# Optimization experiments

Measured on AMD Instinct MI355X. Metric: run time of the kernel, lower is better.

Reference implementation:

```python
import jax, jax.numpy as jnp
import numpy as np

N, C, H, W = 1024, 16, 32, 32
E = 4096


def setup_inputs() -> dict:
    key = jax.random.key(0)
    ks = jax.random.split(key, 10)
    feats = jax.random.normal(ks[0], (N, C, H, W), dtype=jnp.float32)
    src = jax.random.randint(ks[1], (E,), 0, N)
    dst = jax.random.randint(ks[2], (E,), 0, N)
    sign = jax.random.randint(ks[3], (E,), 0, 2) * 2 - 1  # values in {-1, +1}
    edges = jnp.stack([src, sign, dst], axis=1).astype(jnp.int64)
    s = 0.05
    w1 = jax.random.normal(ks[4], (2 * C, 3 * C, 3, 3), dtype=jnp.float32) * s
    b1 = jnp.zeros((2 * C,), dtype=jnp.float32)
    w2 = jax.random.normal(ks[5], (2 * C, 2 * C, 3, 3), dtype=jnp.float32) * s
    b2 = jnp.zeros((2 * C,), dtype=jnp.float32)
    w3 = jax.random.normal(ks[6], (C, 2 * C, 3, 3), dtype=jnp.float32) * s
    b3 = jnp.zeros((C,), dtype=jnp.float32)
    return {"feats": feats, "edges": edges, "w1": w1, "b1": b1,
            "w2": w2, "b2": b2, "w3": w3, "b3": b3}


def _pool_edges(edges, feats, positive):
    # Bidirectional gather + scatter_add over selected edges.
    # Mask-by-zero keeps shapes static (equivalent math to torch.where selection).
    sign = edges[:, 1]
    mask = (sign > 0) if positive else (sign < 0)
    w = mask.astype(feats.dtype)[:, None, None, None]
    src = edges[:, 0]
    dst = edges[:, 2]
    pooled = jnp.zeros_like(feats)
    pooled = pooled.at[dst].add(feats[src] * w)  # src -> dst
    pooled = pooled.at[src].add(feats[dst] * w)  # dst -> src
    return pooled


def _conv(x, w, b):
    y = jax.lax.conv_general_dilated(
        x, w, window_strides=(1, 1), padding=((1, 1), (1, 1)),
        dimension_numbers=("NCHW", "OIHW", "NCHW"))
    return y + b[None, :, None, None]


def _leaky(x):
    return jax.nn.leaky_relu(x, negative_slope=0.1)


def reference(feats, edges, w1, b1, w2, b2, w3, b3):
    pos = _pool_edges(edges, feats, positive=True)
    neg = _pool_edges(edges, feats, positive=False)
    x = jnp.concatenate([feats, pos, neg], axis=1)  # [N, 3C, H, W]
    x = _leaky(_conv(x, w1, b1))
    x = _leaky(_conv(x, w2, b2))
    x = _leaky(_conv(x, w3, b3))
    return x
```

## Files before the change

kernel.cpp:

```cpp
#include <hip/hip_runtime.h>


#define NIMG 1024
#define CHW  16384
#define NEDGE 4096
#define MAXD 64

#define ICP1 56
#define ICP2 40
#define XSZ (34*34*ICP1)
#define WSZ (14*32*32)

#define WG1N (14*32*32)
#define WG2N (9*32*32)
#define WG3N (9*16*32)
#define WGTOT (WG1N+WG2N+WG3N)

typedef __attribute__((ext_vector_type(8))) _Float16 half8;
typedef __attribute__((ext_vector_type(4))) _Float16 half4;
typedef __attribute__((ext_vector_type(4))) float float4v;

__device__ __forceinline__ float leaky(float x) { return x > 0.f ? x : 0.1f * x; }

__global__ __launch_bounds__(256) void prep_kernel(
    const float* __restrict__ feats, _Float16* __restrict__ fcl,
    const int* __restrict__ edges, int* __restrict__ deg, int* __restrict__ adj,
    const float* __restrict__ w1, const float* __restrict__ w2,
    const float* __restrict__ w3, _Float16* __restrict__ wg)
{
    __shared__ int sdeg[NIMG];
    const int b = blockIdx.x, tid = threadIdx.x;
    if (b < NIMG) {
        const int n = b;
        const float* fb = feats + (size_t)n * CHW;
        _Float16*    ob = fcl   + (size_t)n * 1024 * 16;
        const int p0 = tid * 4;
        float4v t[16];
        #pragma unroll
        for (int c = 0; c < 16; ++c) t[c] = *(const float4v*)(fb + (c << 10) + p0);
        #pragma unroll
        for (int u = 0; u < 4; ++u) {
            half8 v0, v1;
            #pragma unroll
            for (int c = 0; c < 8; ++c) { v0[c] = (_Float16)t[c][u]; v1[c] = (_Float16)t[c+8][u]; }
            *(half8*)(ob + (p0+u)*16)     = v0;
            *(half8*)(ob + (p0+u)*16 + 8) = v1;
        }
        return;
    }
    for (int i = tid; i < NIMG; i += 256) sdeg[i] = 0;
    __syncthreads();
    const bool is64 = (edges[1] == 0);
    for (int it = 0; it < NEDGE/256; ++it) {
        const int e = it*256 + tid;
        int s, sg, d;
        if (is64) { s = edges[6*e]; sg = edges[6*e + 2]; d = edges[6*e + 4]; }
        else      { s = edges[3*e]; sg = edges[3*e + 1]; d = edges[3*e + 2]; }
        const int tag_d = (d << 1) | (int)(sg > 0);
        const int tag_s = (s << 1) | (int)(sg > 0);
        int i = atomicAdd(&sdeg[s], 1); if (i < MAXD) adj[(s << 6) + i] = tag_d;
        int j = atomicAdd(&sdeg[d], 1); if (j < MAXD) adj[(d << 6) + j] = tag_s;
    }
    __syncthreads();
    for (int i = tid; i < NIMG; i += 256) deg[i] = sdeg[i];

    for (int t = tid; t < WGTOT; t += 256) {
        _Float16 val = (_Float16)0.f;
        if (t < WG1N) {
            int ks = t >> 10, oc = (t >> 5) & 31, j32 = t & 31;
            int k = ks*32 + j32;
            if (k < 432) { int tap = k / 48, ic = k - tap*48;
                           val = (_Float16)w1[(oc*48 + ic)*9 + tap]; }
        } else if (t < WG1N + WG2N) {
            int u = t - WG1N;
            int ks = u >> 10, oc = (u >> 5) & 31, j32 = u & 31;
            int k = ks*32 + j32;
            int tap = k >> 5, ic = k & 31;
            val = (_Float16)w2[(oc*32 + ic)*9 + tap];
        } else {
            int u = t - (WG1N + WG2N);
            int ks = u >> 9, oc = (u >> 5) & 15, j32 = u & 31;
            int k = ks*32 + j32;
            int tap = k >> 5, ic = k & 31;
            val = (_Float16)w3[(oc*32 + ic)*9 + tap];
        }
        wg[t] = val;
    }
}

__global__ __launch_bounds__(512, 2) void conv_kernel(
    const _Float16* __restrict__ fcl,
    const int* __restrict__ deg, const int* __restrict__ adj,
    const _Float16* __restrict__ wg,
    const float* __restrict__ b1, const float* __restrict__ b2,
    const float* __restrict__ b3, float* __restrict__ out)
{
    __shared__ __align__(16) _Float16 Xs[XSZ];
    __shared__ __align__(16) _Float16 Ws[WSZ];
    const int n    = blockIdx.x;
    const int tid  = threadIdx.x;
    const int wave = tid >> 6;
    const int lane = tid & 63;
    const int col  = lane & 15;
    const int quad = lane >> 4;

    {
        const half8* fc = (const half8*)(fcl + (size_t)n * CHW);
        int m = deg[n]; if (m > MAXD) m = MAXD;
        const int* al = adj + (n << 6);
        #pragma unroll 2
        for (int h = 0; h < 2; ++h) {
            const int p = tid + h*512;
            const int base = (((p >> 5) + 1)*34 + (p & 31) + 1) * ICP1;
            *(half8*)(Xs + base)     = fc[2*p];
            *(half8*)(Xs + base + 8) = fc[2*p + 1];
            float ap[16], an[16];
            #pragma unroll
            for (int c = 0; c < 16; ++c) { ap[c] = 0.f; an[c] = 0.f; }
            int i = 0;
            for (; i + 8 <= m; i += 8) {
                int v[8]; half8 x[16];
                #pragma unroll
                for (int u = 0; u < 8; ++u) v[u] = al[i+u];
                #pragma unroll
                for (int u = 0; u < 8; ++u) {
                    const half8* f = (const half8*)(fcl + (size_t)(v[u] >> 1) * CHW);
                    x[2*u] = f[2*p]; x[2*u+1] = f[2*p+1];
                }
                #pragma unroll
                for (int u = 0; u < 8; ++u) {
                    if (v[u] & 1) { for (int c = 0; c < 8; ++c) { ap[c] += (float)x[2*u][c]; ap[c+8] += (float)x[2*u+1][c]; } }
                    else          { for (int c = 0; c < 8; ++c) { an[c] += (float)x[2*u][c]; an[c+8] += (float)x[2*u+1][c]; } }
                }
            }
            for (; i + 4 <= m; i += 4) {
                int v[4]; half8 x[8];
                #pragma unroll
                for (int u = 0; u < 4; ++u) v[u] = al[i+u];
                #pragma unroll
                for (int u = 0; u < 4; ++u) {
                    const half8* f = (const half8*)(fcl + (size_t)(v[u] >> 1) * CHW);
                    x[2*u] = f[2*p]; x[2*u+1] = f[2*p+1];
                }
                #pragma unroll
                for (int u = 0; u < 4; ++u) {
                    if (v[u] & 1) { for (int c = 0; c < 8; ++c) { ap[c] += (float)x[2*u][c]; ap[c+8] += (float)x[2*u+1][c]; } }
                    else          { for (int c = 0; c < 8; ++c) { an[c] += (float)x[2*u][c]; an[c+8] += (float)x[2*u+1][c]; } }
                }
            }
            for (; i < m; ++i) {
                const int v = al[i];
                const half8* fb = (const half8*)(fcl + (size_t)(v >> 1) * CHW);
                half8 x0 = fb[2*p], x1 = fb[2*p + 1];
                if (v & 1) {
                    #pragma unroll
                    for (int c = 0; c < 8; ++c) { ap[c] += (float)x0[c]; ap[c+8] += (float)x1[c]; }
                } else {
                    #pragma unroll
                    for (int c = 0; c < 8; ++c) { an[c] += (float)x0[c]; an[c+8] += (float)x1[c]; }
                }
            }
            half8 h0, h1, h2, h3;
            #pragma unroll
            for (int c = 0; c < 8; ++c) { h0[c] = (_Float16)ap[c]; h1[c] = (_Float16)ap[c+8];
                                          h2[c] = (_Float16)an[c]; h3[c] = (_Float16)an[c+8]; }
            *(half8*)(Xs + base + 16) = h0;
            *(half8*)(Xs + base + 24) = h1;
            *(half8*)(Xs + base + 32) = h2;
            *(half8*)(Xs + base + 40) = h3;
        }
        {
            const half8* src = (const half8*)wg;
            half8* dst = (half8*)Ws;
            for (int t = tid; t < WG1N/8; t += 512) dst[t] = src[t];
        }
        if (tid < 132) {
            int hp, wp;
            if      (tid < 34)  { hp = 0;        wp = tid; }
            else if (tid < 68)  { hp = 33;       wp = tid - 34; }
            else if (tid < 100) { hp = tid - 67; wp = 0; }
            else                { hp = tid - 99; wp = 33; }
            int hb = (hp*34 + wp) * ICP1;
            #pragma unroll
            for (int t = 0; t < 6; ++t) *(half8*)(Xs + hb + t*8) = (half8)0;
        }
    }
    __syncthreads();

    float4v acc[2][8];

    {
        #pragma unroll
        for (int m = 0; m < 2; ++m)
            #pragma unroll
            for (int j = 0; j < 8; ++j) acc[m][j] = (float4v){0.f,0.f,0.f,0.f};
        int pixb[8];
        #pragma unroll
        for (int j = 0; j < 8; ++j) {
            int p = wave*128 + j*16 + col;
            pixb[j] = ((p >> 5)*34 + (p & 31)) * ICP1;
        }
        const int abase = col*32 + quad*8;
        #pragma unroll
        for (int ks = 0; ks < 14; ++ks) {
            int kq  = ks*32 + quad*8;
            int tap = kq / 48;
            int off = 0;
            if (tap < 9) {
                int ic0 = kq - tap*48;
                int dh = tap / 3, dw = tap - dh*3;
                off = (dh*34 + dw)*ICP1 + ic0;
            }
            half8 a0 = *(const half8*)(Ws + ks*1024 + abase);
            half8 a1 = *(const half8*)(Ws + ks*1024 + 512 + abase);
            #pragma unroll
            for (int j = 0; j < 8; ++j) {
                half8 b = *(const half8*)(Xs + pixb[j] + off);
                acc[0][j] = __builtin_amdgcn_mfma_f32_16x16x32_f16(a0, b, acc[0][j], 0, 0, 0);
                acc[1][j] = __builtin_amdgcn_mfma_f32_16x16x32_f16(a1, b, acc[1][j], 0, 0, 0);
            }
        }
    }
    __syncthreads();

    {
        if (tid < 132) {
            int hp, wp;
            if      (tid < 34)  { hp = 0;        wp = tid; }
            else if (tid < 68)  { hp = 33;       wp = tid - 34; }
            else if (tid < 100) { hp = tid - 67; wp = 0; }
            else                { hp = tid - 99; wp = 33; }
            int hb = (hp*34 + wp) * ICP2;
            #pragma unroll
            for (int t = 0; t < 4; ++t) *(half8*)(Xs + hb + t*8) = (half8)0;
        }
        float bv[2][4];
        #pragma unroll
        for (int m = 0; m < 2; ++m)
            #pragma unroll
            for (int r = 0; r < 4; ++r) bv[m][r] = b1[m*16 + quad*4 + r];
        #pragma unroll
        for (int m = 0; m < 2; ++m)
            #pragma unroll
            for (int j = 0; j < 8; ++j) {
                int p = wave*128 + j*16 + col;
                _Float16* y = Xs + ((((p>>5)+1)*34) + (p&31) + 1)*ICP2 + m*16 + quad*4;
                half4 v;
                #pragma unroll
                for (int r = 0; r < 4; ++r) v[r] = (_Float16)leaky(acc[m][j][r] + bv[m][r]);
                *(half4*)y = v;
            }
        {
            const half8* src = (const half8*)(wg + WG1N);
            half8* dst = (half8*)Ws;
            for (int t = tid; t < WG2N/8; t += 512) dst[t] = src[t];
        }
    }
    __syncthreads();

    {
        #pragma unroll
        for (int m = 0; m < 2; ++m)
            #pragma unroll
            for (int j = 0; j < 8; ++j) acc[m][j] = (float4v){0.f,0.f,0.f,0.f};
        int pixb[8];
        #pragma unroll
        for (int j = 0; j < 8; ++j) {
            int p = wave*128 + j*16 + col;
            pixb[j] = ((p >> 5)*34 + (p & 31)) * ICP2;
        }
        const int abase = col*32 + quad*8;
        #pragma unroll
        for (int ks = 0; ks < 9; ++ks) {
            int kq  = ks*32 + quad*8;
            int tap = kq >> 5, ic0 = kq & 31;
            int dh = tap / 3, dw = tap - dh*3;
            int off = (dh*34 + dw)*ICP2 + ic0;
            half8 a0 = *(const half8*)(Ws + ks*1024 + abase);
            half8 a1 = *(const half8*)(Ws + ks*1024 + 512 + abase);
            #pragma unroll
            for (int j = 0; j < 8; ++j) {
                half8 b = *(const half8*)(Xs + pixb[j] + off);
                acc[0][j] = __builtin_amdgcn_mfma_f32_16x16x32_f16(a0, b, acc[0][j], 0, 0, 0);
                acc[1][j] = __builtin_amdgcn_mfma_f32_16x16x32_f16(a1, b, acc[1][j], 0, 0, 0);
            }
        }
    }
    __syncthreads();

    {
        float bv[2][4];
        #pragma unroll
        for (int m = 0; m < 2; ++m)
            #pragma unroll
            for (int r = 0; r < 4; ++r) bv[m][r] = b2[m*16 + quad*4 + r];
        #pragma unroll
        for (int m = 0; m < 2; ++m)
            #pragma unroll
            for (int j = 0; j < 8; ++j) {
                int p = wave*128 + j*16 + col;
                _Float16* y = Xs + ((((p>>5)+1)*34) + (p&31) + 1)*ICP2 + m*16 + quad*4;
                half4 v;
                #pragma unroll
                for (int r = 0; r < 4; ++r) v[r] = (_Float16)leaky(acc[m][j][r] + bv[m][r]);
                *(half4*)y = v;
            }
        {
            const half8* src = (const half8*)(wg + WG1N + WG2N);
            half8* dst = (half8*)Ws;
            for (int t = tid; t < WG3N/8; t += 512) dst[t] = src[t];
        }
    }
    __syncthreads();

    {
        float4v a3[8];
        #pragma unroll
        for (int j = 0; j < 8; ++j) a3[j] = (float4v){0.f,0.f,0.f,0.f};
        int pixb[8];
        #pragma unroll
        for (int j = 0; j < 8; ++j) {
            int p = wave*128 + j*16 + col;
            pixb[j] = ((p >> 5)*34 + (p & 31)) * ICP2;
        }
        const int abase = col*32 + quad*8;
        #pragma unroll
        for (int ks = 0; ks < 9; ++ks) {
            int kq  = ks*32 + quad*8;
            int tap = kq >> 5, ic0 = kq & 31;
            int dh = tap / 3, dw = tap - dh*3;
            int off = (dh*34 + dw)*ICP2 + ic0;
            half8 a0 = *(const half8*)(Ws + ks*512 + abase);
            #pragma unroll
            for (int j = 0; j < 8; ++j) {
                half8 b = *(const half8*)(Xs + pixb[j] + off);
                a3[j] = __builtin_amdgcn_mfma_f32_16x16x32_f16(a0, b, a3[j], 0, 0, 0);
            }
        }
        float bv[4];
        #pragma unroll
        for (int r = 0; r < 4; ++r) bv[r] = b3[quad*4 + r];
        float* op = out + (size_t)n * CHW;
        #pragma unroll
        for (int j = 0; j < 8; ++j) {
            int p = wave*128 + j*16 + col;
            #pragma unroll
            for (int r = 0; r < 4; ++r)
                op[(quad*4 + r)*1024 + p] = leaky(a3[j][r] + bv[r]);
        }
    }
}

extern "C" void kernel_launch(void* const* d_in, const int* in_sizes, int n_in,
                              void* d_out, int out_size, void* d_ws, size_t ws_size,
                              hipStream_t stream) {
    const float* feats = (const float*)d_in[0];
    const int*   edges = (const int*)  d_in[1];
    const float* w1 = (const float*)d_in[2];
    const float* b1 = (const float*)d_in[3];
    const float* w2 = (const float*)d_in[4];
    const float* b2 = (const float*)d_in[5];
    const float* w3 = (const float*)d_in[6];
    const float* b3 = (const float*)d_in[7];
    float* out = (float*)d_out;

    _Float16* fcl = (_Float16*)d_ws;
    int* deg = (int*)((char*)d_ws + (32u << 20));
    int* adj = deg + NIMG;
    _Float16* wg = (_Float16*)((char*)d_ws + (32u << 20) + 4096 + NIMG*MAXD*4);

    prep_kernel<<<dim3(NIMG + 1), dim3(256), 0, stream>>>(
        feats, fcl, edges, deg, adj, w1, w2, w3, wg);
    conv_kernel<<<dim3(NIMG), dim3(512), 0, stream>>>(fcl, deg, adj, wg,
                                                      b1, b2, b3, out);
}
```

Baseline: 268.2 us.

## Overlap neighbor gather with self-channel conv1 MFMAs and drop weight LDS staging

Reorders the conv1 K dimension so the first five k-steps use only the image's own channels. Those MFMAs now run while the first batch of neighbor gathers is in flight, and the pooled channels are written afterwards. Conv weights are read directly from global memory instead of being staged in LDS, which frees about 28 KB of shared memory. Edge adjacency building is spread over 16 blocks using global atomics after a memset, replacing a single block doing all edges serially. The cost is an extra memset launch, more register pressure from the prefetched gather data, and a small padding increase in conv1 from 14 to 15 k-steps.

After: 221.6 us. 1.21x faster.

```diff
diff --git a/kernel.cpp b/kernel.cpp
--- a/kernel.cpp
+++ b/kernel.cpp
@@ -9,9 +9,9 @@
 #define ICP1 56
 #define ICP2 40
 #define XSZ (34*34*ICP1)
-#define WSZ (14*32*32)
-
-#define WG1N (14*32*32)
+
+#define NK1 15
+#define WG1N (NK1*32*32)
 #define WG2N (9*32*32)
 #define WG3N (9*16*32)
 #define WGTOT (WG1N+WG2N+WG3N)
@@ -28,7 +28,6 @@
     const float* __restrict__ w1, const float* __restrict__ w2,
     const float* __restrict__ w3, _Float16* __restrict__ wg)
 {
-    __shared__ int sdeg[NIMG];
     const int b = blockIdx.x, tid = threadIdx.x;
     if (b < NIMG) {
         const int n = b;
@@ -48,29 +47,23 @@
         }
         return;
     }
-    for (int i = tid; i < NIMG; i += 256) sdeg[i] = 0;
-    __syncthreads();
+    const int e = (b - NIMG) * 256 + tid;
     const bool is64 = (edges[1] == 0);
-    for (int it = 0; it < NEDGE/256; ++it) {
-        const int e = it*256 + tid;
-        int s, sg, d;
-        if (is64) { s = edges[6*e]; sg = edges[6*e + 2]; d = edges[6*e + 4]; }
-        else      { s = edges[3*e]; sg = edges[3*e + 1]; d = edges[3*e + 2]; }
-        const int tag_d = (d << 1) | (int)(sg > 0);
-        const int tag_s = (s << 1) | (int)(sg > 0);
-        int i = atomicAdd(&sdeg[s], 1); if (i < MAXD) adj[(s << 6) + i] = tag_d;
-        int j = atomicAdd(&sdeg[d], 1); if (j < MAXD) adj[(d << 6) + j] = tag_s;
-    }
-    __syncthreads();
-    for (int i = tid; i < NIMG; i += 256) deg[i] = sdeg[i];
-
-    for (int t = tid; t < WGTOT; t += 256) {
+    int s, sg, d;
+    if (is64) { s = edges[6*e]; sg = edges[6*e + 2]; d = edges[6*e + 4]; }
+    else      { s = edges[3*e]; sg = edges[3*e + 1]; d = edges[3*e + 2]; }
+    const int tag_d = (d << 1) | (int)(sg > 0);
+    const int tag_s = (s << 1) | (int)(sg > 0);
+    int i = atomicAdd(&deg[s], 1); if (i < MAXD) adj[(s << 6) + i] = tag_d;
+    int j = atomicAdd(&deg[d], 1); if (j < MAXD) adj[(d << 6) + j] = tag_s;
+
+    for (int t = e; t < WGTOT; t += NEDGE) {
         _Float16 val = (_Float16)0.f;
         if (t < WG1N) {
             int ks = t >> 10, oc = (t >> 5) & 31, j32 = t & 31;
-            int k = ks*32 + j32;
-            if (k < 432) { int tap = k / 48, ic = k - tap*48;
-                           val = (_Float16)w1[(oc*48 + ic)*9 + tap]; }
+            int g = ks / 5, r = (ks - g*5)*32 + j32;
+            int tap = r >> 4, icw = r & 15;
+            if (tap < 9) val = (_Float16)w1[(oc*48 + g*16 + icw)*9 + tap];
         } else if (t < WG1N + WG2N) {
             int u = t - WG1N;
             int ks = u >> 10, oc = (u >> 5) & 31, j32 = u & 31;
@@ -88,6 +81,67 @@
     }
 }
 
+__device__ __forceinline__ void gaccum(
+    const _Float16* __restrict__ fcl, const int* __restrict__ al,
+    int i, int m, int p, float* __restrict__ ap, float* __restrict__ an)
+{
+    for (; i + 8 <= m; i += 8) {
+        int v[8]; half8 x[16];
+        #pragma unroll
+        for (int u = 0; u < 8; ++u) v[u] = al[i+u];
+        #pragma unroll
+        for (int u = 0; u < 8; ++u) {
+            const half8* f = (const half8*)(fcl + (size_t)(v[u] >> 1) * CHW);
+            x[2*u] = f[2*p]; x[2*u+1] = f[2*p+1];
+        }
+        #pragma unroll
+        for (int u = 0; u < 8; ++u) {
+            if (v[u] & 1) { for (int c = 0; c < 8; ++c) { ap[c] += (float)x[2*u][c]; ap[c+8] += (float)x[2*u+1][c]; } }
+            else          { for (int c = 0; c < 8; ++c) { an[c] += (float)x[2*u][c]; an[c+8] += (float)x[2*u+1][c]; } }
+        }
+    }
+    for (; i + 4 <= m; i += 4) {
+        int v[4]; half8 x[8];
+        #pragma unroll
+        for (int u = 0; u < 4; ++u) v[u] = al[i+u];
+        #pragma unroll
+        for (int u = 0; u < 4; ++u) {
+            const half8* f = (const half8*)(fcl + (size_t)(v[u] >> 1) * CHW);
+            x[2*u] = f[2*p]; x[2*u+1] = f[2*p+1];
+        }
+        #pragma unroll
+        for (int u = 0; u < 4; ++u) {
+            if (v[u] & 1) { for (int c = 0; c < 8; ++c) { ap[c] += (float)x[2*u][c]; ap[c+8] += (float)x[2*u+1][c]; } }
+            else          { for (int c = 0; c < 8; ++c) { an[c] += (float)x[2*u][c]; an[c+8] += (float)x[2*u+1][c]; } }
+        }
+    }
+    for (; i < m; ++i) {
+        const int v = al[i];
+        const half8* fb = (const half8*)(fcl + (size_t)(v >> 1) * CHW);
+        half8 x0 = fb[2*p], x1 = fb[2*p + 1];
+        if (v & 1) {
+            #pragma unroll
+            for (int c = 0; c < 8; ++c) { ap[c] += (float)x0[c]; ap[c+8] += (float)x1[c]; }
+        } else {
+            #pragma unroll
+            for (int c = 0; c < 8; ++c) { an[c] += (float)x0[c]; an[c+8] += (float)x1[c]; }
+        }
+    }
+}
+
+__device__ __forceinline__ void pooled_write(
+    _Float16* __restrict__ Xs, int base, const float* ap, const float* an)
+{
+    half8 h0, h1, h2, h3;
+    #pragma unroll
+    for (int c = 0; c < 8; ++c) { h0[c] = (_Float16)ap[c]; h1[c] = (_Float16)ap[c+8];
+                                  h2[c] = (_Float16)an[c]; h3[c] = (_Float16)an[c+8]; }
+    *(half8*)(Xs + base + 16) = h0;
+    *(half8*)(Xs + base + 24) = h1;
+    *(half8*)(Xs + base + 32) = h2;
+    *(half8*)(Xs + base + 40) = h3;
+}
+
 __global__ __launch_bounds__(512, 2) void conv_kernel(
     const _Float16* __restrict__ fcl,
     const int* __restrict__ deg, const int* __restrict__ adj,
@@ -96,129 +150,120 @@
     const float* __restrict__ b3, float* __restrict__ out)
 {
     __shared__ __align__(16) _Float16 Xs[XSZ];
-    __shared__ __align__(16) _Float16 Ws[WSZ];
     const int n    = blockIdx.x;
     const int tid  = threadIdx.x;
     const int wave = tid >> 6;
     const int lane = tid & 63;
     const int col  = lane & 15;
     const int quad = lane >> 4;
-
-    {
-        const half8* fc = (const half8*)(fcl + (size_t)n * CHW);
-        int m = deg[n]; if (m > MAXD) m = MAXD;
-        const int* al = adj + (n << 6);
-        #pragma unroll 2
-        for (int h = 0; h < 2; ++h) {
-            const int p = tid + h*512;
-            const int base = (((p >> 5) + 1)*34 + (p & 31) + 1) * ICP1;
-            *(half8*)(Xs + base)     = fc[2*p];
-            *(half8*)(Xs + base + 8) = fc[2*p + 1];
-            float ap[16], an[16];
-            #pragma unroll
-            for (int c = 0; c < 16; ++c) { ap[c] = 0.f; an[c] = 0.f; }
-            int i = 0;
-            for (; i + 8 <= m; i += 8) {
-                int v[8]; half8 x[16];
-                #pragma unroll
-                for (int u = 0; u < 8; ++u) v[u] = al[i+u];
-                #pragma unroll
-                for (int u = 0; u < 8; ++u) {
-                    const half8* f = (const half8*)(fcl + (size_t)(v[u] >> 1) * CHW);
-                    x[2*u] = f[2*p]; x[2*u+1] = f[2*p+1];
-                }
-                #pragma unroll
-                for (int u = 0; u < 8; ++u) {
-                    if (v[u] & 1) { for (int c = 0; c < 8; ++c) { ap[c] += (float)x[2*u][c]; ap[c+8] += (float)x[2*u+1][c]; } }
-                    else          { for (int c = 0; c < 8; ++c) { an[c] += (float)x[2*u][c]; an[c+8] += (float)x[2*u+1][c]; } }
-                }
+    const int p0 = tid, p1 = tid + 512;
+    const int base0 = (((p0 >> 5) + 1)*34 + (p0 & 31) + 1) * ICP1;
+    const int base1 = (((p1 >> 5) + 1)*34 + (p1 & 31) + 1) * ICP1;
+
+    const _Float16* wg1 = wg;
+    const _Float16* wg2 = wg + WG1N;
+    const _Float16* wg3 = wg + WG1N + WG2N;
+
+    const half8* fc = (const half8*)(fcl + (size_t)n * CHW);
+    int m = deg[n]; if (m > MAXD) m = MAXD;
+    const int* al = adj + (n << 6);
+
+    *(half8*)(Xs + base0)     = fc[2*p0];
+    *(half8*)(Xs + base0 + 8) = fc[2*p0 + 1];
+    *(half8*)(Xs + base1)     = fc[2*p1];
+    *(half8*)(Xs + base1 + 8) = fc[2*p1 + 1];
+    if (tid < 132) {
+        int hp, wp;
+        if      (tid < 34)  { hp = 0;        wp = tid; }
+        else if (tid < 68)  { hp = 33;       wp = tid - 34; }
+        else if (tid < 100) { hp = tid - 67; wp = 0; }
+        else                { hp = tid - 99; wp = 33; }
+        int hb = (hp*34 + wp) * ICP1;
+        #pragma unroll
+        for (int t = 0; t < 6; ++t) *(half8*)(Xs + hb + t*8) = (half8)0;
+    }
+    const int nb = m < 8 ? m : 8;
+    int v0[8]; half8 x0[16];
+    #pragma unroll
+    for (int u = 0; u < 8; ++u)
+        if (u < nb) {
+            v0[u] = al[u];
+            const half8* f = (const half8*)(fcl + (size_t)(v0[u] >> 1) * CHW);
+            x0[2*u] = f[2*p0]; x0[2*u+1] = f[2*p0 + 1];
+        }
+    __syncthreads();
+
+    float4v acc[2][8];
+    #pragma unroll
+    for (int mm = 0; mm < 2; ++mm)
+        #pragma unroll
+        for (int j = 0; j < 8; ++j) acc[mm][j] = (float4v){0.f,0.f,0.f,0.f};
+    int pixb[8];
+    #pragma unroll
+    for (int j = 0; j < 8; ++j) {
+        int p = wave*128 + j*16 + col;
+        pixb[j] = ((p >> 5)*34 + (p & 31)) * ICP1;
+    }
+    const int abase = col*32 + quad*8;
+
+    #pragma unroll
+    for (int ks = 0; ks < 5; ++ks) {
+        int r   = ks*32 + quad*8;
+        int tap = r >> 4;
+        int off = 0;
+        if (tap < 9) {
+            int dh = tap / 3, dw = tap - dh*3;
+            off = (dh*34 + dw)*ICP1 + (r & 15);
+        }
+        half8 a0 = *(const half8*)(wg1 + ks*1024 + abase);
+        half8 a1 = *(const half8*)(wg1 + ks*1024 + 512 + abase);
+        #pragma unroll
+        for (int j = 0; j < 8; ++j) {
+            half8 b = *(const half8*)(Xs + pixb[j] + off);
+            acc[0][j] = __builtin_amdgcn_mfma_f32_16x16x32_f16(a0, b, acc[0][j], 0, 0, 0);
+            acc[1][j] = __builtin_amdgcn_mfma_f32_16x16x32_f16(a1, b, acc[1][j], 0, 0, 0);
+        }
+    }
+
+    {
+        float ap[16], an[16];
+        #pragma unroll
+        for (int c = 0; c < 16; ++c) { ap[c] = 0.f; an[c] = 0.f; }
+        #pragma unroll
+        for (int u = 0; u < 8; ++u)
+            if (u < nb) {
+                if (v0[u] & 1) { for (int c = 0; c < 8; ++c) { ap[c] += (float)x0[2*u][c]; ap[c+8] += (float)x0[2*u+1][c]; } }
+                else           { for (int c = 0; c < 8; ++c) { an[c] += (float)x0[2*u][c]; an[c+8] += (float)x0[2*u+1][c]; } }
             }
-            for (; i + 4 <= m; i += 4) {
-                int v[4]; half8 x[8];
-                #pragma unroll
-                for (int u = 0; u < 4; ++u) v[u] = al[i+u];
-                #pragma unroll
-                for (int u = 0; u < 4; ++u) {
-                    const half8* f = (const half8*)(fcl + (size_t)(v[u] >> 1) * CHW);
-                    x[2*u] = f[2*p]; x[2*u+1] = f[2*p+1];
-                }
-                #pragma unroll
-                for (int u = 0; u < 4; ++u) {
-                    if (v[u] & 1) { for (int c = 0; c < 8; ++c) { ap[c] += (float)x[2*u][c]; ap[c+8] += (float)x[2*u+1][c]; } }
-                    else          { for (int c = 0; c < 8; ++c) { an[c] += (float)x[2*u][c]; an[c+8] += (float)x[2*u+1][c]; } }
-                }
-            }
-            for (; i < m; ++i) {
-                const int v = al[i];
-                const half8* fb = (const half8*)(fcl + (size_t)(v >> 1) * CHW);
-                half8 x0 = fb[2*p], x1 = fb[2*p + 1];
-                if (v & 1) {
-                    #pragma unroll
-                    for (int c = 0; c < 8; ++c) { ap[c] += (float)x0[c]; ap[c+8] += (float)x1[c]; }
-                } else {
-                    #pragma unroll
-                    for (int c = 0; c < 8; ++c) { an[c] += (float)x0[c]; an[c+8] += (float)x1[c]; }
-                }
-            }
-            half8 h0, h1, h2, h3;
-            #pragma unroll
-            for (int c = 0; c < 8; ++c) { h0[c] = (_Float16)ap[c]; h1[c] = (_Float16)ap[c+8];
-                                          h2[c] = (_Float16)an[c]; h3[c] = (_Float16)an[c+8]; }
-            *(half8*)(Xs + base + 16) = h0;
-            *(half8*)(Xs + base + 24) = h1;
-            *(half8*)(Xs + base + 32) = h2;
-            *(half8*)(Xs + base + 40) = h3;
-        }
-        {
-            const half8* src = (const half8*)wg;
-            half8* dst = (half8*)Ws;
-            for (int t = tid; t < WG1N/8; t += 512) dst[t] = src[t];
-        }
-        if (tid < 132) {
-            int hp, wp;
-            if      (tid < 34)  { hp = 0;        wp = tid; }
-            else if (tid < 68)  { hp = 33;       wp = tid - 34; }
-            else if (tid < 100) { hp = tid - 67; wp = 0; }
-            else                { hp = tid - 99; wp = 33; }
-            int hb = (hp*34 + wp) * ICP1;
-            #pragma unroll
-            for (int t = 0; t < 6; ++t) *(half8*)(Xs + hb + t*8) = (half8)0;
-        }
-    }
-    __syncthreads();
-
-    float4v acc[2][8];
-
-    {
-        #pragma unroll
-        for (int m = 0; m < 2; ++m)
-            #pragma unroll
-            for (int j = 0; j < 8; ++j) acc[m][j] = (float4v){0.f,0.f,0.f,0.f};
-        int pixb[8];
+        gaccum(fcl, al, nb, m, p0, ap, an);
+        pooled_write(Xs, base0, ap, an);
+    }
+    {
+        float ap[16], an[16];
+        #pragma unroll
+        for (int c = 0; c < 16; ++c) { ap[c] = 0.f; an[c] = 0.f; }
+        gaccum(fcl, al, 0, m, p1, ap, an);
+        pooled_write(Xs, base1, ap, an);
+    }
+    __syncthreads();
+
+    #pragma unroll
+    for (int ks = 5; ks < NK1; ++ks) {
+        int g   = ks / 5;
+        int r   = (ks - g*5)*32 + quad*8;
+        int tap = r >> 4;
+        int off = 0;
+        if (tap < 9) {
+            int dh = tap / 3, dw = tap - dh*3;
+            off = (dh*34 + dw)*ICP1 + g*16 + (r & 15);
+        }
+        half8 a0 = *(const half8*)(wg1 + ks*1024 + abase);
+        half8 a1 = *(const half8*)(wg1 + ks*1024 + 512 + abase);
         #pragma unroll
         for (int j = 0; j < 8; ++j) {
-            int p = wave*128 + j*16 + col;
-            pixb[j] = ((p >> 5)*34 + (p & 31)) * ICP1;
-        }
-        const int abase = col*32 + quad*8;
-        #pragma unroll
-        for (int ks = 0; ks < 14; ++ks) {
-            int kq  = ks*32 + quad*8;
-            int tap = kq / 48;
-            int off = 0;
-            if (tap < 9) {
-                int ic0 = kq - tap*48;
-                int dh = tap / 3, dw = tap - dh*3;
-                off = (dh*34 + dw)*ICP1 + ic0;
-            }
-            half8 a0 = *(const half8*)(Ws + ks*1024 + abase);
-            half8 a1 = *(const half8*)(Ws + ks*1024 + 512 + abase);
-            #pragma unroll
-            for (int j = 0; j < 8; ++j) {
-                half8 b = *(const half8*)(Xs + pixb[j] + off);
-                acc[0][j] = __builtin_amdgcn_mfma_f32_16x16x32_f16(a0, b, acc[0][j], 0, 0, 0);
-                acc[1][j] = __builtin_amdgcn_mfma_f32_16x16x32_f16(a1, b, acc[1][j], 0, 0, 0);
-            }
+            half8 b = *(const half8*)(Xs + pixb[j] + off);
+            acc[0][j] = __builtin_amdgcn_mfma_f32_16x16x32_f16(a0, b, acc[0][j], 0, 0, 0);
+            acc[1][j] = __builtin_amdgcn_mfma_f32_16x16x32_f16(a1, b, acc[1][j], 0, 0, 0);
         }
     }
     __syncthreads();
@@ -236,51 +281,45 @@
         }
         float bv[2][4];
         #pragma unroll
-        for (int m = 0; m < 2; ++m)
-            #pragma unroll
-            for (int r = 0; r < 4; ++r) bv[m][r] = b1[m*16 + quad*4 + r];
-        #pragma unroll
-        for (int m = 0; m < 2; ++m)
+        for (int mm = 0; mm < 2; ++mm)
+            #pragma unroll
+            for (int r = 0; r < 4; ++r) bv[mm][r] = b1[mm*16 + quad*4 + r];
+        #pragma unroll
+        for (int mm = 0; mm < 2; ++mm)
             #pragma unroll
             for (int j = 0; j < 8; ++j) {
                 int p = wave*128 + j*16 + col;
-                _Float16* y = Xs + ((((p>>5)+1)*34) + (p&31) + 1)*ICP2 + m*16 + quad*4;
+                _Float16* y = Xs + ((((p>>5)+1)*34) + (p&31) + 1)*ICP2 + mm*16 + quad*4;
                 half4 v;
                 #pragma unroll
-                for (int r = 0; r < 4; ++r) v[r] = (_Float16)leaky(acc[m][j][r] + bv[m][r]);
+                for (int r = 0; r < 4; ++r) v[r] = (_Float16)leaky(acc[mm][j][r] + bv[mm][r]);
                 *(half4*)y = v;
             }
-        {
-            const half8* src = (const half8*)(wg + WG1N);
-            half8* dst = (half8*)Ws;
-            for (int t = tid; t < WG2N/8; t += 512) dst[t] = src[t];
-        }
-    }
-    __syncthreads();
-
-    {
-        #pragma unroll
-        for (int m = 0; m < 2; ++m)
-            #pragma unroll
-            for (int j = 0; j < 8; ++j) acc[m][j] = (float4v){0.f,0.f,0.f,0.f};
-        int pixb[8];
+    }
+    __syncthreads();
+
+    {
+        #pragma unroll
+        for (int mm = 0; mm < 2; ++mm)
+            #pragma unroll
+            for (int j = 0; j < 8; ++j) acc[mm][j] = (float4v){0.f,0.f,0.f,0.f};
+        int pxb[8];
         #pragma unroll
         for (int j = 0; j < 8; ++j) {
             int p = wave*128 + j*16 + col;
-            pixb[j] = ((p >> 5)*34 + (p & 31)) * ICP2;
-        }
-        const int abase = col*32 + quad*8;
+            pxb[j] = ((p >> 5)*34 + (p & 31)) * ICP2;
+        }
         #pragma unroll
         for (int ks = 0; ks < 9; ++ks) {
             int kq  = ks*32 + quad*8;
             int tap = kq >> 5, ic0 = kq & 31;
             int dh = tap / 3, dw = tap - dh*3;
             int off = (dh*34 + dw)*ICP2 + ic0;
-            half8 a0 = *(const half8*)(Ws + ks*1024 + abase);
-            half8 a1 = *(const half8*)(Ws + ks*1024 + 512 + abase);
+            half8 a0 = *(const half8*)(wg2 + ks*1024 + abase);
+            half8 a1 = *(const half8*)(wg2 + ks*1024 + 512 + abase);
             #pragma unroll
             for (int j = 0; j < 8; ++j) {
-                half8 b = *(const half8*)(Xs + pixb[j] + off);
+                half8 b = *(const half8*)(Xs + pxb[j] + off);
                 acc[0][j] = __builtin_amdgcn_mfma_f32_16x16x32_f16(a0, b, acc[0][j], 0, 0, 0);
                 acc[1][j] = __builtin_amdgcn_mfma_f32_16x16x32_f16(a1, b, acc[1][j], 0, 0, 0);
             }
@@ -291,25 +330,20 @@
     {
         float bv[2][4];
         #pragma unroll
-        for (int m = 0; m < 2; ++m)
-            #pragma unroll
-            for (int r = 0; r < 4; ++r) bv[m][r] = b2[m*16 + quad*4 + r];
-        #pragma unroll
-        for (int m = 0; m < 2; ++m)
+        for (int mm = 0; mm < 2; ++mm)
+            #pragma unroll
+            for (int r = 0; r < 4; ++r) bv[mm][r] = b2[mm*16 + quad*4 + r];
+        #pragma unroll
+        for (int mm = 0; mm < 2; ++mm)
             #pragma unroll
             for (int j = 0; j < 8; ++j) {
                 int p = wave*128 + j*16 + col;
-                _Float16* y = Xs + ((((p>>5)+1)*34) + (p&31) + 1)*ICP2 + m*16 + quad*4;
+                _Float16* y = Xs + ((((p>>5)+1)*34) + (p&31) + 1)*ICP2 + mm*16 + quad*4;
                 half4 v;
                 #pragma unroll
-                for (int r = 0; r < 4; ++r) v[r] = (_Float16)leaky(acc[m][j][r] + bv[m][r]);
+                for (int r = 0; r < 4; ++r) v[r] = (_Float16)leaky(acc[mm][j][r] + bv[mm][r]);
                 *(half4*)y = v;
             }
-        {
-            const half8* src = (const half8*)(wg + WG1N + WG2N);
-            half8* dst = (half8*)Ws;
-            for (int t = tid; t < WG3N/8; t += 512) dst[t] = src[t];
-        }
     }
     __syncthreads();
 
@@ -317,23 +351,22 @@
         float4v a3[8];
         #pragma unroll
         for (int j = 0; j < 8; ++j) a3[j] = (float4v){0.f,0.f,0.f,0.f};
-        int pixb[8];
+        int pxb[8];
         #pragma unroll
         for (int j = 0; j < 8; ++j) {
             int p = wave*128 + j*16 + col;
-            pixb[j] = ((p >> 5)*34 + (p & 31)) * ICP2;
-        }
-        const int abase = col*32 + quad*8;
+            pxb[j] = ((p >> 5)*34 + (p & 31)) * ICP2;
+        }
         #pragma unroll
         for (int ks = 0; ks < 9; ++ks) {
             int kq  = ks*32 + quad*8;
             int tap = kq >> 5, ic0 = kq & 31;
             int dh = tap / 3, dw = tap - dh*3;
             int off = (dh*34 + dw)*ICP2 + ic0;
-            half8 a0 = *(const half8*)(Ws + ks*512 + abase);
+            half8 a0 = *(const half8*)(wg3 + ks*512 + abase);
             #pragma unroll
             for (int j = 0; j < 8; ++j) {
-                half8 b = *(const half8*)(Xs + pixb[j] + off);
+                half8 b = *(const half8*)(Xs + pxb[j] + off);
                 a3[j] = __builtin_amdgcn_mfma_f32_16x16x32_f16(a0, b, a3[j], 0, 0, 0);
             }
         }
@@ -369,7 +402,8 @@
     int* adj = deg + NIMG;
     _Float16* wg = (_Float16*)((char*)d_ws + (32u << 20) + 4096 + NIMG*MAXD*4);
 
-    prep_kernel<<<dim3(NIMG + 1), dim3(256), 0, stream>>>(
+    hipMemsetAsync(deg, 0, NIMG * sizeof(int), stream);
+    prep_kernel<<<dim3(NIMG + NEDGE/256), dim3(256), 0, stream>>>(
         feats, fcl, edges, deg, adj, w1, w2, w3, wg);
     conv_kernel<<<dim3(NIMG), dim3(512), 0, stream>>>(fcl, deg, adj, wg,
                                                       b1, b2, b3, out);
```
